# Performance work log

Measured on AMD Instinct MI355X. Metric: run time of the kernel, lower is better.

## Reference

```python
import jax, jax.numpy as jnp
import numpy as np

B, T, D = 16, 512, 384
MAX_DUR = 8          # durations drawn from [0, MAX_DUR)
OUT_LEN = T * (MAX_DUR - 1)  # static upper bound on total expanded length
PAD_VALUE = 0.0


def setup_inputs() -> dict:
    key = jax.random.key(0)
    k1, k2, k3 = jax.random.split(key, 3)
    xs = jax.random.normal(k1, (B, T, D), dtype=jnp.float32)
    ds = jax.random.randint(k2, (B, T), 0, MAX_DUR, dtype=jnp.int32)
    ilens = jax.random.randint(k3, (B,), T // 2, T + 1, dtype=jnp.int32)
    return {"xs": xs, "ds": ds, "ilens": ilens}


def reference(xs, ds, ilens):
    # Zero out durations past each sequence's valid length (equiv. to x[:ilen], d[:ilen]).
    t_src = jnp.arange(T, dtype=jnp.int32)
    d_eff = jnp.where(t_src[None, :] < ilens[:, None], ds, 0)        # (B, T)
    csum = jnp.cumsum(d_eff, axis=1)                                 # (B, T) inclusive cumsum
    total = csum[:, -1]                                              # (B,) expanded lengths

    # For each output frame t, source index i is smallest i with csum[i] > t.
    t_out = jnp.arange(OUT_LEN, dtype=jnp.int32)                     # (OUT_LEN,)
    idx = jax.vmap(lambda c: jnp.searchsorted(c, t_out, side="right"))(csum)  # (B, OUT_LEN)
    idx = jnp.minimum(idx, T - 1)

    out = jnp.take_along_axis(xs, idx[:, :, None], axis=1)           # (B, OUT_LEN, D)
    valid = t_out[None, :] < total[:, None]                          # (B, OUT_LEN)
    return jnp.where(valid[:, :, None], out, jnp.asarray(PAD_VALUE, xs.dtype))
```

## Files before the change

### kernel.cpp

```cpp
#include <hip/hip_runtime.h>

#define B_SZ 16
#define T_SZ 512
#define D_SZ 384
#define MAX_DUR 8
#define OUT_LEN (T_SZ * (MAX_DUR - 1))
#define D4 (D_SZ / 4)
#define TOTAL4 (B_SZ * OUT_LEN * D4)

__global__ void __launch_bounds__(T_SZ) scan_search_kernel(
    const int* __restrict__ ds,
    const int* __restrict__ ilens,
    int* __restrict__ idx_out)
{
    __shared__ int s[T_SZ];
    const int b = blockIdx.x;
    const int t = threadIdx.x;
    const int ilen = ilens[b];

    int val = (t < ilen) ? ds[b * T_SZ + t] : 0;
    s[t] = val;
    __syncthreads();

    #pragma unroll
    for (int off = 1; off < T_SZ; off <<= 1) {
        int add = (t >= off) ? s[t - off] : 0;
        __syncthreads();
        s[t] += add;
        __syncthreads();
    }

    const int total = s[T_SZ - 1];

    for (int k = t; k < OUT_LEN; k += T_SZ) {
        int lo = 0, hi = T_SZ;
        while (lo < hi) {
            int mid = (lo + hi) >> 1;
            if (s[mid] <= k) lo = mid + 1; else hi = mid;
        }
        int idx = lo < (T_SZ - 1) ? lo : (T_SZ - 1);
        idx_out[b * OUT_LEN + k] = (k < total) ? idx : -1;
    }
}

__global__ void __launch_bounds__(256) gather_kernel(
    const float4* __restrict__ xs,
    const int* __restrict__ idx,
    float4* __restrict__ out)
{
    int gid = blockIdx.x * 256 + threadIdx.x;
    if (gid >= TOTAL4) return;

    int row = gid / D4;
    int d4  = gid - row * D4;
    int i   = idx[row];

    float4 v;
    if (i < 0) {
        v.x = 0.f; v.y = 0.f; v.z = 0.f; v.w = 0.f;
    } else {
        int b = row / OUT_LEN;
        v = xs[(b * T_SZ + i) * D4 + d4];
    }
    out[gid] = v;
}

extern "C" void kernel_launch(void* const* d_in, const int* in_sizes, int n_in,
                              void* d_out, int out_size, void* d_ws, size_t ws_size,
                              hipStream_t stream) {
    const float* xs    = (const float*)d_in[0];
    const int*   ds    = (const int*)d_in[1];
    const int*   ilens = (const int*)d_in[2];
    float*       out   = (float*)d_out;
    int*         idx   = (int*)d_ws;

    scan_search_kernel<<<B_SZ, T_SZ, 0, stream>>>(ds, ilens, idx);

    constexpr int nblk = (TOTAL4 + 255) / 256;
    gather_kernel<<<nblk, 256, 0, stream>>>(
        (const float4*)xs, idx, (float4*)out);
}
```

Baseline: 110.3 us.

## Replace binary-search scan with wave-shuffle scan plus scatter; batch gather with nontemporal stores

The scan kernel now uses wavefront shuffle prefix sums and a per-wave total combine, then each source index scatters itself into a shared output-index table instead of every output frame binary-searching the cumsum. The gather kernel handles four float4 elements per thread and issues its loads before its stores. Padded rows load from a clamped index and are then zeroed, and output writes use nontemporal stores to avoid polluting cache. The main cost being targeted is the store-bound gather of roughly 88MB, where the gains from unrolling and nontemporal stores are uncertain, and the scan kernel is small.

```diff
diff --git a/kernel.cpp b/kernel.cpp
--- a/kernel.cpp
+++ b/kernel.cpp
@@ -7,62 +7,90 @@
 #define OUT_LEN (T_SZ * (MAX_DUR - 1))
 #define D4 (D_SZ / 4)
 #define TOTAL4 (B_SZ * OUT_LEN * D4)
+#define NWAVE (T_SZ / 64)
+#define NPT 4
+#define GBLK 256
 
-__global__ void __launch_bounds__(T_SZ) scan_search_kernel(
+typedef float vfloat4 __attribute__((ext_vector_type(4)));
+
+__global__ void __launch_bounds__(T_SZ) scan_scatter_kernel(
     const int* __restrict__ ds,
     const int* __restrict__ ilens,
     int* __restrict__ idx_out)
 {
-    __shared__ int s[T_SZ];
-    const int b = blockIdx.x;
-    const int t = threadIdx.x;
+    __shared__ int wsum[NWAVE];
+    __shared__ int sidx[OUT_LEN];
+    const int b    = blockIdx.x;
+    const int t    = threadIdx.x;
+    const int lane = t & 63;
+    const int w    = t >> 6;
     const int ilen = ilens[b];
+    const int val  = (t < ilen) ? ds[b * T_SZ + t] : 0;
 
-    int val = (t < ilen) ? ds[b * T_SZ + t] : 0;
-    s[t] = val;
+    int x = val;
+    #pragma unroll
+    for (int off = 1; off < 64; off <<= 1) {
+        int y = __shfl_up(x, off);
+        if (lane >= off) x += y;
+    }
+    if (lane == 63) wsum[w] = x;
+    __syncthreads();
+
+    int prev = 0, tot = 0;
+    #pragma unroll
+    for (int i = 0; i < NWAVE; ++i) {
+        int wsv = wsum[i];
+        tot += wsv;
+        if (i < w) prev += wsv;
+    }
+    const int end   = x + prev;
+    const int start = end - val;
+
+    for (int r = start; r < end; ++r) sidx[r] = t;
     __syncthreads();
 
     #pragma unroll
-    for (int off = 1; off < T_SZ; off <<= 1) {
-        int add = (t >= off) ? s[t - off] : 0;
-        __syncthreads();
-        s[t] += add;
-        __syncthreads();
-    }
-
-    const int total = s[T_SZ - 1];
-
-    for (int k = t; k < OUT_LEN; k += T_SZ) {
-        int lo = 0, hi = T_SZ;
-        while (lo < hi) {
-            int mid = (lo + hi) >> 1;
-            if (s[mid] <= k) lo = mid + 1; else hi = mid;
-        }
-        int idx = lo < (T_SZ - 1) ? lo : (T_SZ - 1);
-        idx_out[b * OUT_LEN + k] = (k < total) ? idx : -1;
+    for (int k = 0; k < OUT_LEN / T_SZ; ++k) {
+        int o = k * T_SZ + t;
+        idx_out[b * OUT_LEN + o] = (o < tot) ? sidx[o] : -1;
     }
 }
 
-__global__ void __launch_bounds__(256) gather_kernel(
-    const float4* __restrict__ xs,
+static_assert(TOTAL4 % (GBLK * NPT) == 0, "grid must tile exactly");
+
+__global__ void __launch_bounds__(GBLK) gather_kernel(
+    const vfloat4* __restrict__ xs,
     const int* __restrict__ idx,
-    float4* __restrict__ out)
+    vfloat4* __restrict__ out)
 {
-    int gid = blockIdx.x * 256 + threadIdx.x;
-    if (gid >= TOTAL4) return;
+    const int base = blockIdx.x * (GBLK * NPT) + threadIdx.x;
 
-    int row = gid / D4;
-    int d4  = gid - row * D4;
-    int i   = idx[row];
+    int g[NPT], row[NPT], d4v[NPT];
+    #pragma unroll
+    for (int j = 0; j < NPT; ++j) {
+        g[j]   = base + j * GBLK;
+        row[j] = g[j] / D4;
+        d4v[j] = g[j] - row[j] * D4;
+    }
 
-    float4 v;
-    if (i < 0) {
-        v.x = 0.f; v.y = 0.f; v.z = 0.f; v.w = 0.f;
-    } else {
-        int b = row / OUT_LEN;
-        v = xs[(b * T_SZ + i) * D4 + d4];
+    int src[NPT];
+    #pragma unroll
+    for (int j = 0; j < NPT; ++j) src[j] = idx[row[j]];
+
+    vfloat4 v[NPT];
+    #pragma unroll
+    for (int j = 0; j < NPT; ++j) {
+        int bb = row[j] / OUT_LEN;
+        int ii = src[j] < 0 ? 0 : src[j];
+        v[j] = xs[(bb * T_SZ + ii) * D4 + d4v[j]];
     }
-    out[gid] = v;
+
+    #pragma unroll
+    for (int j = 0; j < NPT; ++j) {
+        vfloat4 zero = (vfloat4)0.0f;
+        vfloat4 r = src[j] < 0 ? zero : v[j];
+        __builtin_nontemporal_store(r, &out[g[j]]);
+    }
 }
 
 extern "C" void kernel_launch(void* const* d_in, const int* in_sizes, int n_in,
@@ -74,9 +102,9 @@
     float*       out   = (float*)d_out;
     int*         idx   = (int*)d_ws;
 
-    scan_search_kernel<<<B_SZ, T_SZ, 0, stream>>>(ds, ilens, idx);
+    scan_scatter_kernel<<<B_SZ, T_SZ, 0, stream>>>(ds, ilens, idx);
 
-    constexpr int nblk = (TOTAL4 + 255) / 256;
-    gather_kernel<<<nblk, 256, 0, stream>>>(
-        (const float4*)xs, idx, (float4*)out);
+    constexpr int nblk = TOTAL4 / (GBLK * NPT);
+    gather_kernel<<<nblk, GBLK, 0, stream>>>(
+        (const vfloat4*)xs, idx, (vfloat4*)out);
 }
```

Result: no change. 111.2 us (+0.8%).

## Fuse scan and search into gather kernel with per-block redundant scan

Applied to the files above, without the earlier changes.

Merges the two-kernel pipeline into one launch. Each gather block recomputes the batch's duration cumsum using wave shuffles and then binary-searches only the output rows it covers. Each thread now copies four float4 elements and uses nontemporal stores. This removes a kernel launch, the global index buffer and the dependency between the two kernels. The cost is a redundant 512-element scan and extra barriers in every one of roughly 5k blocks.

```diff
diff --git a/kernel.cpp b/kernel.cpp
--- a/kernel.cpp
+++ b/kernel.cpp
@@ -6,77 +6,101 @@
 #define MAX_DUR 8
 #define OUT_LEN (T_SZ * (MAX_DUR - 1))
 #define D4 (D_SZ / 4)
-#define TOTAL4 (B_SZ * OUT_LEN * D4)
+#define ROW4_PER_B (OUT_LEN * D4)
+#define TOTAL4 (B_SZ * ROW4_PER_B)
+#define BLK 256
+#define NPT 4
+#define F4_PER_BLK (BLK * NPT)
+#define BLK_PER_B (ROW4_PER_B / F4_PER_BLK)
+#define NBLK (B_SZ * BLK_PER_B)
+#define NWAVE (BLK / 64)
+#define MAXROWS 12
 
-__global__ void __launch_bounds__(T_SZ) scan_search_kernel(
+typedef float vfloat4 __attribute__((ext_vector_type(4)));
+
+static_assert(ROW4_PER_B % F4_PER_BLK == 0, "block must not straddle batches");
+
+__global__ void __launch_bounds__(BLK) fused_regularizer_kernel(
+    const vfloat4* __restrict__ xs,
     const int* __restrict__ ds,
     const int* __restrict__ ilens,
-    int* __restrict__ idx_out)
+    vfloat4* __restrict__ out)
 {
-    __shared__ int s[T_SZ];
-    const int b = blockIdx.x;
-    const int t = threadIdx.x;
-    const int ilen = ilens[b];
+    __shared__ int scsum[T_SZ];
+    __shared__ int swsum[NWAVE];
+    __shared__ int sfr[MAXROWS];
 
-    int val = (t < ilen) ? ds[b * T_SZ + t] : 0;
-    s[t] = val;
+    const int t        = threadIdx.x;
+    const int lane     = t & 63;
+    const int w        = t >> 6;
+    const int batch    = blockIdx.x / BLK_PER_B;
+    const int blk_in_b = blockIdx.x - batch * BLK_PER_B;
+    const int base4    = blk_in_b * F4_PER_BLK;
+
+    const int ilen = ilens[batch];
+    const int p0 = 2 * t, p1 = 2 * t + 1;
+    const int e0 = (p0 < ilen) ? ds[batch * T_SZ + p0] : 0;
+    const int e1 = (p1 < ilen) ? ds[batch * T_SZ + p1] : 0;
+    const int p  = e0 + e1;
+
+    int x = p;
+    #pragma unroll
+    for (int off = 1; off < 64; off <<= 1) {
+        int y = __shfl_up(x, off);
+        if (lane >= off) x += y;
+    }
+    if (lane == 63) swsum[w] = x;
     __syncthreads();
 
+    int prev = 0, tot = 0;
     #pragma unroll
-    for (int off = 1; off < T_SZ; off <<= 1) {
-        int add = (t >= off) ? s[t - off] : 0;
-        __syncthreads();
-        s[t] += add;
-        __syncthreads();
+    for (int i = 0; i < NWAVE; ++i) {
+        int v = swsum[i];
+        tot += v;
+        if (i < w) prev += v;
     }
+    const int excl = x - p + prev;
+    scsum[p0] = excl + e0;
+    scsum[p1] = excl + e0 + e1;
+    __syncthreads();
 
-    const int total = s[T_SZ - 1];
-
-    for (int k = t; k < OUT_LEN; k += T_SZ) {
+    const int rstart = base4 / D4;
+    const int rend   = (base4 + F4_PER_BLK - 1) / D4;
+    if (t <= rend - rstart) {
+        const int k = rstart + t;
         int lo = 0, hi = T_SZ;
         while (lo < hi) {
             int mid = (lo + hi) >> 1;
-            if (s[mid] <= k) lo = mid + 1; else hi = mid;
+            if (scsum[mid] <= k) lo = mid + 1; else hi = mid;
         }
         int idx = lo < (T_SZ - 1) ? lo : (T_SZ - 1);
-        idx_out[b * OUT_LEN + k] = (k < total) ? idx : -1;
+        sfr[t] = (k < tot) ? idx : -1;
     }
-}
+    __syncthreads();
 
-__global__ void __launch_bounds__(256) gather_kernel(
-    const float4* __restrict__ xs,
-    const int* __restrict__ idx,
-    float4* __restrict__ out)
-{
-    int gid = blockIdx.x * 256 + threadIdx.x;
-    if (gid >= TOTAL4) return;
+    const vfloat4* __restrict__ xb = xs + (size_t)batch * T_SZ * D4;
+    vfloat4* __restrict__ ob       = out + (size_t)batch * ROW4_PER_B + base4;
 
-    int row = gid / D4;
-    int d4  = gid - row * D4;
-    int i   = idx[row];
-
-    float4 v;
-    if (i < 0) {
-        v.x = 0.f; v.y = 0.f; v.z = 0.f; v.w = 0.f;
-    } else {
-        int b = row / OUT_LEN;
-        v = xs[(b * T_SZ + i) * D4 + d4];
+    #pragma unroll
+    for (int j = 0; j < NPT; ++j) {
+        const int g   = j * BLK + t;
+        const int gg  = base4 + g;
+        const int row = gg / D4;
+        const int d4  = gg - row * D4;
+        const int i   = sfr[row - rstart];
+        vfloat4 v = xb[(i < 0 ? 0 : i) * D4 + d4];
+        vfloat4 z = (vfloat4)0.0f;
+        __builtin_nontemporal_store(i < 0 ? z : v, &ob[g]);
     }
-    out[gid] = v;
 }
 
 extern "C" void kernel_launch(void* const* d_in, const int* in_sizes, int n_in,
                               void* d_out, int out_size, void* d_ws, size_t ws_size,
                               hipStream_t stream) {
-    const float* xs    = (const float*)d_in[0];
-    const int*   ds    = (const int*)d_in[1];
-    const int*   ilens = (const int*)d_in[2];
-    float*       out   = (float*)d_out;
-    int*         idx   = (int*)d_ws;
+    const vfloat4* xs  = (const vfloat4*)d_in[0];
+    const int* ds      = (const int*)d_in[1];
+    const int* ilens   = (const int*)d_in[2];
+    vfloat4* out       = (vfloat4*)d_out;
 
-    scan_search_kernel<<<B_SZ, T_SZ, 0, stream>>>(ds, ilens, idx);
-
-    constexpr int nblk = (TOTAL4 + 255) / 256;
-    gather_kernel<<<nblk, 256, 0, stream>>>(
-        (const float4*)xs, idx, (float4*)out);
+    fused_regularizer_kernel<<<NBLK, BLK, 0, stream>>>(xs, ds, ilens, out);
 }
```

Result: no change. 109.5 us (-0.7%).
